# Kernel tuning notes

Hardware: AMD Instinct MI355X
Metric: run time of the kernel (lower is better)

Reference implementation:

```python
import jax, jax.numpy as jnp
import numpy as np

VOCAB = 1024
EMBED = 256
HIDDEN = 512
MAX_LEN = 32
TEMP = 1.0
BATCH = 2048


def setup_inputs() -> dict:
    key = jax.random.key(0)
    ks = jax.random.split(key, 11)
    s = 0.02  # small init scale for weights
    return dict(
        x=jax.random.normal(ks[0], (BATCH, HIDDEN), dtype=jnp.float32),
        gumbel=jax.random.gumbel(ks[1], (MAX_LEN, BATCH, VOCAB), dtype=jnp.float32),
        W_ih=jax.random.normal(ks[2], (4 * HIDDEN, EMBED), dtype=jnp.float32) * s,
        W_hh=jax.random.normal(ks[3], (4 * HIDDEN, HIDDEN), dtype=jnp.float32) * s,
        b_ih=jax.random.normal(ks[4], (4 * HIDDEN,), dtype=jnp.float32) * s,
        b_hh=jax.random.normal(ks[5], (4 * HIDDEN,), dtype=jnp.float32) * s,
        W_out=jax.random.normal(ks[6], (VOCAB, HIDDEN), dtype=jnp.float32) * s,
        b_out=jax.random.normal(ks[7], (VOCAB,), dtype=jnp.float32) * s,
        W_emb=jax.random.normal(ks[8], (EMBED, VOCAB), dtype=jnp.float32) * s,
        b_emb=jax.random.normal(ks[9], (EMBED,), dtype=jnp.float32) * s,
        sos=jax.random.normal(ks[10], (EMBED,), dtype=jnp.float32) * 0.01,
    )


def reference(x, gumbel, W_ih, W_hh, b_ih, b_hh, W_out, b_out, W_emb, b_emb, sos):
    B = x.shape[0]
    h0 = x                                   # prev_hidden = input features
    c0 = jnp.zeros_like(x)
    e0 = jnp.broadcast_to(sos, (B, EMBED))   # SOS embedding

    def step(carry, g):
        h, c, e = carry
        # torch LSTMCell gate order: i, f, g, o
        gates = e @ W_ih.T + b_ih + h @ W_hh.T + b_hh   # [B, 4H]
        i, f, gg, o = jnp.split(gates, 4, axis=-1)
        i = jax.nn.sigmoid(i)
        f = jax.nn.sigmoid(f)
        gg = jnp.tanh(gg)
        o = jax.nn.sigmoid(o)
        c_new = f * c + i * gg
        h_new = o * jnp.tanh(c_new)
        logits = h_new @ W_out.T + b_out                # [B, V]
        # RelaxedOneHotCategorical rsample: softmax((logits + Gumbel)/temp)
        x_s = jax.nn.softmax((logits + g) / TEMP, axis=-1)
        e_new = x_s @ W_emb.T + b_emb                   # [B, E]
        return (h_new, c_new, e_new), x_s

    _, seq = jax.lax.scan(step, (h0, c0, e0), gumbel)   # [L, B, V]
    seq = jnp.transpose(seq, (1, 0, 2))                 # [B, L, V]
    eos = jnp.zeros((B, 1, VOCAB), seq.dtype).at[:, 0, 0].set(1.0)
    return jnp.concatenate([seq, eos], axis=1)          # [B, L+1, V]
```

## Files before the change

kernel.cpp:

```cpp
#include <hip/hip_runtime.h>
#include <hip/hip_bf16.h>

#define B_   2048
#define V_   1024
#define H_   512
#define E_   256
#define L_   32

typedef __attribute__((ext_vector_type(4))) float f32x4;
typedef unsigned short u16;
typedef unsigned int   u32;
typedef unsigned char  u8;
typedef unsigned long long u64;
typedef long long      i64;

__device__ __forceinline__ u32 f32b(float x){ union{float f;u32 u;}v; v.f=x; return v.u; }
__device__ __forceinline__ float bf32(u32 u){ union{float f;u32 u;}v; v.u=u; return v.f; }
__device__ __forceinline__ u16 f2bf(float x) {
    u32 u = f32b(x);
    u32 r = u + 0x7fffu + ((u >> 16) & 1u);
    return (u16)(r >> 16);
}
__device__ __forceinline__ u8 f2e4m3(float x) {
    u32 u = f32b(x);
    u32 s = (u >> 24) & 0x80u;
    u32 a = u & 0x7fffffffu;
    if (a < 0x3c800000u) return (u8)s;
    if (a > 0x43e00000u) a = 0x43e00000u;
    u32 r = a + 0x000fffffu + ((a >> 20) & 1u);
    if (r > 0x43e00000u) r = 0x43e00000u;
    u32 ex = (r >> 23) - 120u;
    u32 mn = (r >> 20) & 7u;
    return (u8)(s | (ex << 3) | mn);
}
__device__ __forceinline__ u8 f2fp8(float x) {
#if __has_builtin(__builtin_amdgcn_cvt_pk_fp8_f32)
    return (u8)(__builtin_amdgcn_cvt_pk_fp8_f32(x, x, 0, false) & 0xff);
#else
    return f2e4m3(x);
#endif
}
__device__ __forceinline__ float sig_(float x)  { return 1.f / (1.f + __expf(-x)); }
__device__ __forceinline__ float tanh_(float x) { return 1.f - 2.f / (__expf(2.f * x) + 1.f); }

__device__ __forceinline__ void ag_st64(void* p, u64 v) {
    __hip_atomic_store((u64*)p, v, __ATOMIC_RELAXED, __HIP_MEMORY_SCOPE_AGENT);
}
__device__ __forceinline__ u64 ag_ld64(const void* p) {
    return __hip_atomic_load((const u64*)p, __ATOMIC_RELAXED, __HIP_MEMORY_SCOPE_AGENT);
}
__device__ __forceinline__ void ag_st32(void* p, u32 v) {
    __hip_atomic_store((u32*)p, v, __ATOMIC_RELAXED, __HIP_MEMORY_SCOPE_AGENT);
}
__device__ __forceinline__ u32 ag_ld32(const void* p) {
    return __hip_atomic_load((const u32*)p, __ATOMIC_RELAXED, __HIP_MEMORY_SCOPE_AGENT);
}

__global__ void prep(const float* __restrict__ W_ih, const float* __restrict__ W_hh,
                     const float* __restrict__ b_ih, const float* __restrict__ b_hh,
                     const float* __restrict__ W_out, const float* __restrict__ W_emb,
                     u8* __restrict__ w1f, u8* __restrict__ wof, u8* __restrict__ wef,
                     float* __restrict__ b1, u32* __restrict__ flg)
{
    int idx = blockIdx.x * 256 + threadIdx.x;
    if (idx < 1572864) {
        int e = idx & 7, l = (idx >> 3) & 63, jj = (idx >> 9) & 1, wv = (idx >> 10) & 7,
            g = (idx >> 13) & 3;
        int rest = idx >> 15;
        int hb = rest / 24, ks = rest % 24;
        int k = ks * 32 + ((l >> 4) << 3) + e;
        int row = g * 512 + hb * 256 + wv * 32 + jj * 16 + (l & 15);
        float v = (k < E_) ? W_ih[row * E_ + k] : W_hh[row * H_ + (k - E_)];
        w1f[idx] = f2e4m3(v * 64.f);
    } else if (idx < 2097152) {
        int j = idx - 1572864;
        int e = j & 7, l = (j >> 3) & 63, jj = (j >> 9) & 1, wv = (j >> 10) & 7,
            vh2 = (j >> 13) & 1, ks = (j >> 14) & 15, hb = j >> 18;
        int k = ks * 32 + ((l >> 4) << 3) + e;
        int v = hb * 512 + vh2 * 256 + wv * 32 + jj * 16 + (l & 15);
        wof[j] = f2e4m3(W_out[v * H_ + k] * 64.f);
    } else if (idx < 2359296) {
        int j = idx - 2097152;
        int e = j & 7, l = (j >> 3) & 63, jj = (j >> 9) & 1, wv = (j >> 10) & 7,
            ksp = (j >> 13) & 15, hb = j >> 17;
        int kv = hb * 512 + ksp * 32 + ((l >> 4) << 3) + e;
        int ce = wv * 32 + jj * 16 + (l & 15);
        wef[j] = f2e4m3(W_emb[ce * V_ + kv] * 64.f);
    } else if (idx < 2361344) {
        int j = idx - 2359296;
        b1[j] = b_ih[j] + b_hh[j];
    } else if (idx < 2365440) {
        flg[idx - 2361344] = 0u;
    }
}

#define AEO   131072u
#define XSO   143488u
#define RMX   151808u
#define RSM   152320u
#define LDS_TOTAL 152832

#define WAITVM_(N) asm volatile("s_waitcnt vmcnt(" #N ")" ::: "memory")
#define WAITVM(N) WAITVM_(N)

typedef const __attribute__((address_space(1))) void* gvp;
typedef __attribute__((address_space(3))) void* svp;

__device__ __forceinline__ void pbar(u32* myf, u32* pef, u32 n, u32 tid) {
    asm volatile("s_waitcnt vmcnt(0)" ::: "memory");
    __syncthreads();
    if (tid == 0) {
        __hip_atomic_fetch_add(myf, 1u, __ATOMIC_RELAXED, __HIP_MEMORY_SCOPE_AGENT);
        while (__hip_atomic_load(pef, __ATOMIC_RELAXED, __HIP_MEMORY_SCOPE_AGENT) < n)
            __builtin_amdgcn_s_sleep(2);
    }
    __syncthreads();
}

__global__ __launch_bounds__(512, 2)
void lstm_fused(const float* __restrict__ x, const float* __restrict__ gum,
                const u8* __restrict__ w1f, const u8* __restrict__ wof,
                const u8* __restrict__ wef, const float* __restrict__ b1,
                const float* __restrict__ b_out, const float* __restrict__ b_emb,
                const float* __restrict__ sos, float* __restrict__ out,
                u8* __restrict__ hx, char* __restrict__ ms, char* __restrict__ ep,
                u32* __restrict__ flg)
{
    extern __shared__ char smem[];

    const u32 tid = threadIdx.x;
    const u32 w   = tid >> 6;
    const u32 l   = tid & 63u;
    const u32 q   = l >> 4;
    const u32 col = l & 15u;

    const u32 bid = blockIdx.x;
    const u32 p   = bid & 127u;
    const u32 hb  = bid >> 7;
    const u32 ph  = 1u - hb;
    const int r0  = (int)(p << 4);

    u32* myf = flg + p * 32u + hb * 16u;
    u32* pef = flg + p * 32u + ph * 16u;
    u32 nbar = 0;

    const u32 wK  = w << 10;
    const u32 lB  = l << 4;
    const u32 l8  = l << 3;
    const u32 q8  = q << 3;
    const u32 colB776 = col * 776u;
    const u32 colB520 = col * 520u;

    const char* w1p = (const char*)w1f + (size_t)hb * 786432u;
    const char* wop = (const char*)wof + (size_t)hb * 262144u;
    const char* wep = (const char*)wef + (size_t)hb * 131072u;

#define ISS(BASE, C) do { u32 _c = (u32)(C); \
    u32 _o = (u32)__builtin_amdgcn_readfirstlane((int)(((_c & 15u) << 13) + wK)); \
    __builtin_amdgcn_global_load_lds((gvp)((BASE) + ((size_t)_c << 13) + wK + lB), \
                                     (svp)(smem + _o), 16, 0, 0); } while (0)

#define CONSA(G, C) { const char* _fb = smem + (((u32)(C) & 15u) << 13) + wK + l8; \
    acc[G][0] = __builtin_amdgcn_mfma_f32_16x16x32_fp8_fp8(a8, *(const i64*)(_fb), acc[G][0], 0, 0, 0); \
    acc[G][1] = __builtin_amdgcn_mfma_f32_16x16x32_fp8_fp8(a8, *(const i64*)(_fb + 512u), acc[G][1], 0, 0, 0); }

#define CONSB(V2, C, A8) { const char* _fb = smem + (((u32)(C) & 15u) << 13) + wK + l8; \
    accB[V2][0] = __builtin_amdgcn_mfma_f32_16x16x32_fp8_fp8(A8, *(const i64*)(_fb), accB[V2][0], 0, 0, 0); \
    accB[V2][1] = __builtin_amdgcn_mfma_f32_16x16x32_fp8_fp8(A8, *(const i64*)(_fb + 512u), accB[V2][1], 0, 0, 0); }

#define CONSC(C) { const char* _fb = smem + (((u32)(C) & 15u) << 13) + wK + l8; \
    i64 _x = *(const i64*)(smem + XSO + colB520 + (((u32)(C)) << 5) + q8); \
    accC[0] = __builtin_amdgcn_mfma_f32_16x16x32_fp8_fp8(_x, *(const i64*)(_fb), accC[0], 0, 0, 0); \
    accC[1] = __builtin_amdgcn_mfma_f32_16x16x32_fp8_fp8(_x, *(const i64*)(_fb + 512u), accC[1], 0, 0, 0); }

    for (u32 i = tid; i < 16u * 512u; i += 512u) {
        u32 row = i >> 9, vl = i & 511u;
        __builtin_nontemporal_store((hb == 0u && vl == 0u) ? 1.f : 0.f,
            &out[((size_t)(r0 + (int)row) * 33 + 32) * V_ + hb * 512u + vl]);
    }
    for (u32 i = tid; i < 16u * 256u; i += 512u) {
        u32 row = i >> 8, k = i & 255u;
        *(u8*)(smem + AEO + row * 776u + k) = f2fp8(sos[k] * 16.f);
    }
    for (u32 i = tid; i < 16u * 512u; i += 512u) {
        u32 row = i >> 9, k = i & 511u;
        *(u8*)(smem + AEO + row * 776u + 256u + k) = f2fp8(x[(r0 + (int)row) * H_ + k] * 16.f);
    }

    float bia[2], bfa[2], bga[2], boa[2];
    #pragma unroll
    for (int jj = 0; jj < 2; ++jj) {
        int jg = (int)(hb * 256u + (w << 5) + ((u32)jj << 4) + col);
        bia[jj] = b1[jg];           bfa[jj] = b1[H_ + jg];
        bga[jj] = b1[2 * H_ + jg];  boa[jj] = b1[3 * H_ + jg];
    }
    float bov[2][2];
    #pragma unroll
    for (int v2 = 0; v2 < 2; ++v2)
        #pragma unroll
        for (int jj = 0; jj < 2; ++jj)
            bov[v2][jj] = b_out[hb * 512u + (u32)v2 * 256u + (w << 5) + ((u32)jj << 4) + col];
    float bem16[2];
    #pragma unroll
    for (int jj = 0; jj < 2; ++jj)
        bem16[jj] = b_emb[(w << 5) + ((u32)jj << 4) + col] * 16.f;

    float creg[2][4];
    #pragma unroll
    for (int jj = 0; jj < 2; ++jj)
        #pragma unroll
        for (int r = 0; r < 4; ++r) creg[jj][r] = 0.f;

    __syncthreads();

    const f32x4 fz = {0.f, 0.f, 0.f, 0.f};
    const float S1 = 1.f / 1024.f;

    #pragma unroll 1
    for (int t = 0; t < L_; ++t) {
        f32x4 acc[4][2];
        #pragma unroll
        for (int g = 0; g < 4; ++g) { acc[g][0] = fz; acc[g][1] = fz; }

        ISS(w1p, 0);  ISS(w1p, 1);  ISS(w1p, 2);  ISS(w1p, 3);  ISS(w1p, 4);
        ISS(w1p, 5);  ISS(w1p, 6);  ISS(w1p, 7);  ISS(w1p, 8);  ISS(w1p, 9);
        ISS(w1p, 10); ISS(w1p, 11); ISS(w1p, 12); ISS(w1p, 13); ISS(w1p, 14);
        #pragma unroll 1
        for (int ks = 0; ks < 20; ++ks) {
            i64 a8 = *(const i64*)(smem + AEO + colB776 + ((u32)ks << 5) + q8);
            int c0 = ks << 2;
            WAITVM(11);
            CONSA(0, c0); CONSA(1, c0 + 1); CONSA(2, c0 + 2); CONSA(3, c0 + 3);
            ISS(w1p, c0 + 15); ISS(w1p, c0 + 16); ISS(w1p, c0 + 17); ISS(w1p, c0 + 18);
        }
        {   i64 a8 = *(const i64*)(smem + AEO + colB776 + (20u << 5) + q8);
            WAITVM(11); CONSA(0, 80); CONSA(1, 81); CONSA(2, 82); CONSA(3, 83); ISS(w1p, 95); }
        {   i64 a8 = *(const i64*)(smem + AEO + colB776 + (21u << 5) + q8);
            WAITVM(8);  CONSA(0, 84); CONSA(1, 85); CONSA(2, 86); CONSA(3, 87); }
        {   i64 a8 = *(const i64*)(smem + AEO + colB776 + (22u << 5) + q8);
            WAITVM(4);  CONSA(0, 88); CONSA(1, 89); CONSA(2, 90); CONSA(3, 91); }
        {   i64 a8 = *(const i64*)(smem + AEO + colB776 + (23u << 5) + q8);
            WAITVM(0);  CONSA(0, 92); CONSA(1, 93); CONSA(2, 94); CONSA(3, 95); }
        __syncthreads();

        #pragma unroll
        for (int jj = 0; jj < 2; ++jj) {
            u32 jg = hb * 256u + (w << 5) + ((u32)jj << 4) + col;
            #pragma unroll
            for (int r = 0; r < 4; ++r) {
                float gi = sig_(acc[0][jj][r] * S1 + bia[jj]);
                float gf = sig_(acc[1][jj][r] * S1 + bfa[jj]);
                float gg = tanh_(acc[2][jj][r] * S1 + bga[jj]);
                float go = sig_(acc[3][jj][r] * S1 + boa[jj]);
                float c  = gf * creg[jj][r] + gi * gg;
                creg[jj][r] = c;
                float h = go * tanh_(c);
                *(u8*)(smem + AEO + ((q << 2) + (u32)r) * 776u + 256u + jg) = f2fp8(h * 16.f);
            }
        }
        __syncthreads();

        {   u32 row = tid >> 5, off = (tid & 31u) << 3;
            u64 v = *(const u64*)(smem + AEO + row * 776u + 256u + hb * 256u + off);
            ag_st64(hx + (size_t)p * 8192u + row * 512u + hb * 256u + off, v);
        }
        ++nbar; pbar(myf, pef, nbar, tid);
        {   u32 row = tid >> 5, off = (tid & 31u) << 3;
            u64 v = ag_ld64(hx + (size_t)p * 8192u + row * 512u + ph * 256u + off);
            *(u64*)(smem + AEO + row * 776u + 256u + ph * 256u + off) = v;
        }
        __syncthreads();

        const float* gt = gum + (size_t)t * (B_ * V_) + (size_t)r0 * V_;
        float gr[2][2][4];
        #pragma unroll
        for (int v2 = 0; v2 < 2; ++v2)
            #pragma unroll
            for (int jj = 0; jj < 2; ++jj) {
                u32 vg = hb * 512u + (u32)v2 * 256u + (w << 5) + ((u32)jj << 4) + col;
                #pragma unroll
                for (int r = 0; r < 4; ++r)
                    gr[v2][jj][r] = __builtin_nontemporal_load(&gt[((q << 2) + (u32)r) * V_ + vg]);
            }

        f32x4 accB[2][2];
        accB[0][0] = fz; accB[0][1] = fz; accB[1][0] = fz; accB[1][1] = fz;
        ISS(wop, 0);  ISS(wop, 1);  ISS(wop, 2);  ISS(wop, 3);  ISS(wop, 4);
        ISS(wop, 5);  ISS(wop, 6);  ISS(wop, 7);  ISS(wop, 8);  ISS(wop, 9);
        ISS(wop, 10); ISS(wop, 11); ISS(wop, 12); ISS(wop, 13); ISS(wop, 14);
        #pragma unroll 1
        for (int g = 0; g < 4; ++g) {
            i64 a80 = *(const i64*)(smem + AEO + colB776 + 256u + (((u32)g << 1) << 5) + q8);
            i64 a81 = *(const i64*)(smem + AEO + colB776 + 256u + ((((u32)g << 1) | 1u) << 5) + q8);
            int c0 = g << 2;
            WAITVM(11);
            CONSB(0, c0, a80); CONSB(1, c0 + 1, a80);
            CONSB(0, c0 + 2, a81); CONSB(1, c0 + 3, a81);
            ISS(wop, c0 + 15); ISS(wop, c0 + 16); ISS(wop, c0 + 17); ISS(wop, c0 + 18);
        }
        {   i64 a80 = *(const i64*)(smem + AEO + colB776 + 256u + (8u << 5) + q8);
            i64 a81 = *(const i64*)(smem + AEO + colB776 + 256u + (9u << 5) + q8);
            WAITVM(11); CONSB(0, 16, a80); CONSB(1, 17, a80); CONSB(0, 18, a81); CONSB(1, 19, a81);
            ISS(wop, 31); }
        {   i64 a80 = *(const i64*)(smem + AEO + colB776 + 256u + (10u << 5) + q8);
            i64 a81 = *(const i64*)(smem + AEO + colB776 + 256u + (11u << 5) + q8);
            WAITVM(8);  CONSB(0, 20, a80); CONSB(1, 21, a80); CONSB(0, 22, a81); CONSB(1, 23, a81); }
        {   i64 a80 = *(const i64*)(smem + AEO + colB776 + 256u + (12u << 5) + q8);
            i64 a81 = *(const i64*)(smem + AEO + colB776 + 256u + (13u << 5) + q8);
            WAITVM(4);  CONSB(0, 24, a80); CONSB(1, 25, a80); CONSB(0, 26, a81); CONSB(1, 27, a81); }
        {   i64 a80 = *(const i64*)(smem + AEO + colB776 + 256u + (14u << 5) + q8);
            i64 a81 = *(const i64*)(smem + AEO + colB776 + 256u + (15u << 5) + q8);
            WAITVM(0);  CONSB(0, 28, a80); CONSB(1, 29, a80); CONSB(0, 30, a81); CONSB(1, 31, a81); }

        float m_loc[4], s_loc[4];
        #pragma unroll
        for (int r = 0; r < 4; ++r) m_loc[r] = -1e30f;
        #pragma unroll
        for (int v2 = 0; v2 < 2; ++v2)
            #pragma unroll
            for (int jj = 0; jj < 2; ++jj)
                #pragma unroll
                for (int r = 0; r < 4; ++r) {
                    float zz = accB[v2][jj][r] * S1 + bov[v2][jj] + gr[v2][jj][r];
                    accB[v2][jj][r] = zz;
                    m_loc[r] = fmaxf(m_loc[r], zz);
                }
        #pragma unroll
        for (int m = 1; m < 16; m <<= 1)
            #pragma unroll
            for (int r = 0; r < 4; ++r) m_loc[r] = fmaxf(m_loc[r], __shfl_xor(m_loc[r], m, 64));
        if (col == 0) {
            #pragma unroll
            for (int r = 0; r < 4; ++r)
                *(float*)(smem + RMX + ((((q << 2) + (u32)r) << 3) + w) * 4u) = m_loc[r];
        }
        __syncthreads();
        #pragma unroll
        for (int r = 0; r < 4; ++r) {
            float mm = -1e30f;
            #pragma unroll
            for (int ww = 0; ww < 8; ++ww)
                mm = fmaxf(mm, *(const float*)(smem + RMX + ((((q << 2) + (u32)r) << 3) + (u32)ww) * 4u));
            m_loc[r] = mm;
        }
        float ps[4] = {0.f, 0.f, 0.f, 0.f};
        #pragma unroll
        for (int v2 = 0; v2 < 2; ++v2)
            #pragma unroll
            for (int jj = 0; jj < 2; ++jj)
                #pragma unroll
                for (int r = 0; r < 4; ++r) {
                    float Ee = __expf(accB[v2][jj][r] - m_loc[r]);
                    accB[v2][jj][r] = Ee;
                    ps[r] += Ee;
                }
        #pragma unroll
        for (int m = 1; m < 16; m <<= 1)
            #pragma unroll
            for (int r = 0; r < 4; ++r) ps[r] += __shfl_xor(ps[r], m, 64);
        if (col == 0) {
            #pragma unroll
            for (int r = 0; r < 4; ++r)
                *(float*)(smem + RSM + ((((q << 2) + (u32)r) << 3) + w) * 4u) = ps[r];
        }
        __syncthreads();
        #pragma unroll
        for (int r = 0; r < 4; ++r) {
            float ss = 0.f;
            #pragma unroll
            for (int ww = 0; ww < 8; ++ww)
                ss += *(const float*)(smem + RSM + ((((q << 2) + (u32)r) << 3) + (u32)ww) * 4u);
            s_loc[r] = ss;
        }
        if (w == 0 && col == 0) {
            #pragma unroll
            for (int r = 0; r < 4; ++r) {
                u64 v = ((u64)f32b(s_loc[r]) << 32) | (u64)f32b(m_loc[r]);
                ag_st64(ms + (size_t)p * 256u + hb * 128u + (((q << 2) + (u32)r) << 3), v);
            }
        }
        ++nbar; pbar(myf, pef, nbar, tid);
        float fc[4], invs[4];
        #pragma unroll
        for (int r = 0; r < 4; ++r) {
            u64 v = ag_ld64(ms + (size_t)p * 256u + ph * 128u + (((q << 2) + (u32)r) << 3));
            float m_p = bf32((u32)v), s_p = bf32((u32)(v >> 32));
            float mg = fmaxf(m_loc[r], m_p);
            float f0 = __expf(m_loc[r] - mg);
            float s  = s_loc[r] * f0 + s_p * __expf(m_p - mg);
            fc[r] = f0; invs[r] = 1.f / s;
        }
        #pragma unroll
        for (int v2 = 0; v2 < 2; ++v2)
            #pragma unroll
            for (int jj = 0; jj < 2; ++jj) {
                u32 vl = (u32)v2 * 256u + (w << 5) + ((u32)jj << 4) + col;
                u32 vg = hb * 512u + vl;
                #pragma unroll
                for (int r = 0; r < 4; ++r) {
                    float Ee = accB[v2][jj][r] * fc[r];
                    *(u8*)(smem + XSO + ((q << 2) + (u32)r) * 520u + vl) = f2fp8(Ee * 256.f);
                    __builtin_nontemporal_store(Ee * invs[r],
                        &out[((size_t)(r0 + (int)((q << 2) + (u32)r)) * 33 + t) * V_ + vg]);
                }
            }
        __syncthreads();

        f32x4 accC[2];
        accC[0] = fz; accC[1] = fz;
        ISS(wep, 0);  ISS(wep, 1);  ISS(wep, 2);  ISS(wep, 3);  ISS(wep, 4);
        ISS(wep, 5);  ISS(wep, 6);  ISS(wep, 7);  ISS(wep, 8);  ISS(wep, 9);
        ISS(wep, 10); ISS(wep, 11); ISS(wep, 12); ISS(wep, 13); ISS(wep, 14);
        WAITVM(11); CONSC(0);  CONSC(1);  CONSC(2);  CONSC(3);  ISS(wep, 15);
        WAITVM(8);  CONSC(4);  CONSC(5);  CONSC(6);  CONSC(7);
        WAITVM(4);  CONSC(8);  CONSC(9);  CONSC(10); CONSC(11);
        WAITVM(0);  CONSC(12); CONSC(13); CONSC(14); CONSC(15);

        float part[2][4];
        #pragma unroll
        for (int jj = 0; jj < 2; ++jj)
            #pragma unroll
            for (int r = 0; r < 4; ++r)
                part[jj][r] = accC[jj][r] * invs[r] * (16.f / 16384.f);
        #pragma unroll
        for (int r = 0; r < 4; ++r) {
            u32 row = (q << 2) + (u32)r;
            u32 pv = (u32)f2bf(part[0][r]) | ((u32)f2bf(part[1][r]) << 16);
            ag_st32(ep + (size_t)p * 16384u + hb * 8192u + (((row << 3) + w) << 6) + (col << 2), pv);
        }
        ++nbar; pbar(myf, pef, nbar, tid);
        #pragma unroll
        for (int r = 0; r < 4; ++r) {
            u32 row = (q << 2) + (u32)r;
            u32 pv = ag_ld32(ep + (size_t)p * 16384u + ph * 8192u + (((row << 3) + w) << 6) + (col << 2));
            #pragma unroll
            for (int jj = 0; jj < 2; ++jj) {
                float pe = bf32(((pv >> (16 * jj)) & 0xffffu) << 16);
                float e16 = part[jj][r] + pe + bem16[jj];
                *(u8*)(smem + AEO + row * 776u + (w << 5) + ((u32)jj << 4) + col) = f2fp8(e16);
            }
        }
        __syncthreads();
    }
#undef ISS
#undef CONSA
#undef CONSB
#undef CONSC
}

extern "C" void kernel_launch(void* const* d_in, const int* in_sizes, int n_in,
                              void* d_out, int out_size, void* d_ws, size_t ws_size,
                              hipStream_t stream) {
    const float* x     = (const float*)d_in[0];
    const float* gum   = (const float*)d_in[1];
    const float* W_ih  = (const float*)d_in[2];
    const float* W_hh  = (const float*)d_in[3];
    const float* b_ih  = (const float*)d_in[4];
    const float* b_hh  = (const float*)d_in[5];
    const float* W_out = (const float*)d_in[6];
    const float* b_out = (const float*)d_in[7];
    const float* W_emb = (const float*)d_in[8];
    const float* b_emb = (const float*)d_in[9];
    const float* sos   = (const float*)d_in[10];
    float* out = (float*)d_out;

    char* ws = (char*)d_ws;
    u8*    w1f = (u8*)(ws);
    u8*    wof = (u8*)(ws + 1572864);
    u8*    wef = (u8*)(ws + 2097152);
    float* b1  = (float*)(ws + 2359296);
    u32*   flg = (u32*)(ws + 2367488);
    u8*    hx  = (u8*)(ws + 2383872);
    char*  ms  = (char*)(ws + 3432448);
    char*  ep  = (char*)(ws + 3465216);

    hipFuncSetAttribute((const void*)lstm_fused,
                        hipFuncAttributeMaxDynamicSharedMemorySize, LDS_TOTAL);

    prep<<<9240, 256, 0, stream>>>(W_ih, W_hh, b_ih, b_hh, W_out, W_emb,
                                   w1f, wof, wef, b1, flg);
    lstm_fused<<<256, 512, LDS_TOTAL, stream>>>(x, gum, w1f, wof, wef, b1,
                                                b_out, b_emb, sos, out,
                                                hx, ms, ep, flg);
}
```

Baseline: 962.2 us.

## Repartition LSTM across 4 blocks per 32-row group with a weight ring buffer

Each batch group now covers 32 rows split across 4 cooperating blocks instead of 16 rows across 2. Each block holds a quarter of the gate, output and embedding weights and reuses every weight fragment for two row tiles. Weights stream through a 12-slot LDS ring, and the next step's W1 prefetch is issued before the inter-block barrier. The softmax normalisation is deferred so one barrier per step replaces two, at the cost of a 4-way flag and partial-sum exchange.

```diff
diff --git a/kernel.cpp b/kernel.cpp
--- a/kernel.cpp
+++ b/kernel.cpp
@@ -62,60 +62,56 @@
                      u8* __restrict__ w1f, u8* __restrict__ wof, u8* __restrict__ wef,
                      float* __restrict__ b1, u32* __restrict__ flg)
 {
-    int idx = blockIdx.x * 256 + threadIdx.x;
-    if (idx < 1572864) {
-        int e = idx & 7, l = (idx >> 3) & 63, jj = (idx >> 9) & 1, wv = (idx >> 10) & 7,
-            g = (idx >> 13) & 3;
-        int rest = idx >> 15;
-        int hb = rest / 24, ks = rest % 24;
-        int k = ks * 32 + ((l >> 4) << 3) + e;
-        int row = g * 512 + hb * 256 + wv * 32 + jj * 16 + (l & 15);
-        float v = (k < E_) ? W_ih[row * E_ + k] : W_hh[row * H_ + (k - E_)];
+    u32 idx = blockIdx.x * 256 + threadIdx.x;
+    if (idx < 1572864u) {
+        u32 qb = idx / 393216u;
+        u32 r1 = idx - qb * 393216u;
+        u32 ks2 = r1 >> 15;
+        u32 r2 = r1 & 32767u;
+        u32 g = r2 >> 13, wv = (r2 >> 10) & 7u, s = (r2 >> 9) & 1u,
+            l = (r2 >> 3) & 63u, e = r2 & 7u;
+        u32 k = (2u * ks2 + s) * 32u + ((l >> 4) << 3) + e;
+        u32 n = g * 512u + qb * 128u + wv * 16u + (l & 15u);
+        float v = (k < E_) ? W_ih[n * E_ + k] : W_hh[n * H_ + (k - E_)];
         w1f[idx] = f2e4m3(v * 64.f);
-    } else if (idx < 2097152) {
-        int j = idx - 1572864;
-        int e = j & 7, l = (j >> 3) & 63, jj = (j >> 9) & 1, wv = (j >> 10) & 7,
-            vh2 = (j >> 13) & 1, ks = (j >> 14) & 15, hb = j >> 18;
-        int k = ks * 32 + ((l >> 4) << 3) + e;
-        int v = hb * 512 + vh2 * 256 + wv * 32 + jj * 16 + (l & 15);
+    } else if (idx < 2097152u) {
+        u32 j = idx - 1572864u;
+        u32 qb = j >> 17;
+        u32 rem = j & 131071u;
+        u32 ks = rem >> 13, wv = (rem >> 10) & 7u, jv = (rem >> 9) & 1u,
+            l = (rem >> 3) & 63u, e = rem & 7u;
+        u32 k = ks * 32u + ((l >> 4) << 3) + e;
+        u32 v = qb * 256u + wv * 32u + jv * 16u + (l & 15u);
         wof[j] = f2e4m3(W_out[v * H_ + k] * 64.f);
-    } else if (idx < 2359296) {
-        int j = idx - 2097152;
-        int e = j & 7, l = (j >> 3) & 63, jj = (j >> 9) & 1, wv = (j >> 10) & 7,
-            ksp = (j >> 13) & 15, hb = j >> 17;
-        int kv = hb * 512 + ksp * 32 + ((l >> 4) << 3) + e;
-        int ce = wv * 32 + jj * 16 + (l & 15);
+    } else if (idx < 2359296u) {
+        u32 j = idx - 2097152u;
+        u32 qb = j >> 16;
+        u32 rem = j & 65535u;
+        u32 ksp = rem >> 13, wv = (rem >> 10) & 7u, jc = (rem >> 9) & 1u,
+            l = (rem >> 3) & 63u, e = rem & 7u;
+        u32 kv = qb * 256u + ksp * 32u + ((l >> 4) << 3) + e;
+        u32 ce = wv * 32u + jc * 16u + (l & 15u);
         wef[j] = f2e4m3(W_emb[ce * V_ + kv] * 64.f);
-    } else if (idx < 2361344) {
-        int j = idx - 2359296;
+    } else if (idx < 2361344u) {
+        u32 j = idx - 2359296u;
         b1[j] = b_ih[j] + b_hh[j];
-    } else if (idx < 2365440) {
-        flg[idx - 2361344] = 0u;
+    } else if (idx < 2365440u) {
+        flg[idx - 2361344u] = 0u;
     }
 }
 
-#define AEO   131072u
-#define XSO   143488u
-#define RMX   151808u
-#define RSM   152320u
-#define LDS_TOTAL 152832
+#define RING  0u
+#define AEO   98304u
+#define XSO   123136u
+#define RMX   131584u
+#define RSM   132608u
+#define LDS_TOTAL 133632
 
 #define WAITVM_(N) asm volatile("s_waitcnt vmcnt(" #N ")" ::: "memory")
 #define WAITVM(N) WAITVM_(N)
 
 typedef const __attribute__((address_space(1))) void* gvp;
 typedef __attribute__((address_space(3))) void* svp;
-
-__device__ __forceinline__ void pbar(u32* myf, u32* pef, u32 n, u32 tid) {
-    asm volatile("s_waitcnt vmcnt(0)" ::: "memory");
-    __syncthreads();
-    if (tid == 0) {
-        __hip_atomic_fetch_add(myf, 1u, __ATOMIC_RELAXED, __HIP_MEMORY_SCOPE_AGENT);
-        while (__hip_atomic_load(pef, __ATOMIC_RELAXED, __HIP_MEMORY_SCOPE_AGENT) < n)
-            __builtin_amdgcn_s_sleep(2);
-    }
-    __syncthreads();
-}
 
 __global__ __launch_bounds__(512, 2)
 void lstm_fused(const float* __restrict__ x, const float* __restrict__ gum,
@@ -135,86 +131,107 @@
     const u32 col = l & 15u;
 
     const u32 bid = blockIdx.x;
-    const u32 p   = bid & 127u;
-    const u32 hb  = bid >> 7;
-    const u32 ph  = 1u - hb;
-    const int r0  = (int)(p << 4);
-
-    u32* myf = flg + p * 32u + hb * 16u;
-    u32* pef = flg + p * 32u + ph * 16u;
+    const u32 p   = bid & 63u;
+    const u32 qb  = bid >> 6;
+    const u32 q1  = (qb + 1u) & 3u, q2 = (qb + 2u) & 3u, q3 = (qb + 3u) & 3u;
+    const int r0  = (int)(p << 5);
+
+    u32* myf = flg + p * 64u + qb * 16u;
+    u32* pf0 = flg + p * 64u + q1 * 16u;
+    u32* pf1 = flg + p * 64u + q2 * 16u;
+    u32* pf2 = flg + p * 64u + q3 * 16u;
     u32 nbar = 0;
 
-    const u32 wK  = w << 10;
-    const u32 lB  = l << 4;
-    const u32 l8  = l << 3;
-    const u32 q8  = q << 3;
-    const u32 colB776 = col * 776u;
-    const u32 colB520 = col * 520u;
-
-    const char* w1p = (const char*)w1f + (size_t)hb * 786432u;
-    const char* wop = (const char*)wof + (size_t)hb * 262144u;
-    const char* wep = (const char*)wef + (size_t)hb * 131072u;
-
-#define ISS(BASE, C) do { u32 _c = (u32)(C); \
-    u32 _o = (u32)__builtin_amdgcn_readfirstlane((int)(((_c & 15u) << 13) + wK)); \
-    __builtin_amdgcn_global_load_lds((gvp)((BASE) + ((size_t)_c << 13) + wK + lB), \
+    const u32 wK = w << 10, lB = l << 4, l8 = l << 3, q8 = q << 3;
+    const char* w1q = (const char*)w1f + (size_t)qb * 393216u;
+    const char* woq = (const char*)wof + (size_t)qb * 131072u;
+    const char* weq = (const char*)wef + (size_t)qb * 65536u;
+
+#define PBAR() do { WAITVM(0); __syncthreads(); \
+    if (tid == 0) { \
+        __hip_atomic_fetch_add(myf, 1u, __ATOMIC_RELAXED, __HIP_MEMORY_SCOPE_AGENT); \
+        for (;;) { \
+            u32 _a = __hip_atomic_load(pf0, __ATOMIC_RELAXED, __HIP_MEMORY_SCOPE_AGENT); \
+            u32 _b = __hip_atomic_load(pf1, __ATOMIC_RELAXED, __HIP_MEMORY_SCOPE_AGENT); \
+            u32 _c = __hip_atomic_load(pf2, __ATOMIC_RELAXED, __HIP_MEMORY_SCOPE_AGENT); \
+            if (_a >= nbar && _b >= nbar && _c >= nbar) break; \
+            __builtin_amdgcn_s_sleep(2); \
+        } \
+    } \
+    __syncthreads(); } while (0)
+
+#define ISSR(BASE, GOFF, SOFF) do { \
+    u32 _o = (u32)__builtin_amdgcn_readfirstlane((int)((SOFF) + wK)); \
+    __builtin_amdgcn_global_load_lds((gvp)((BASE) + (size_t)(GOFF) + wK + lB), \
                                      (svp)(smem + _o), 16, 0, 0); } while (0)
-
-#define CONSA(G, C) { const char* _fb = smem + (((u32)(C) & 15u) << 13) + wK + l8; \
-    acc[G][0] = __builtin_amdgcn_mfma_f32_16x16x32_fp8_fp8(a8, *(const i64*)(_fb), acc[G][0], 0, 0, 0); \
-    acc[G][1] = __builtin_amdgcn_mfma_f32_16x16x32_fp8_fp8(a8, *(const i64*)(_fb + 512u), acc[G][1], 0, 0, 0); }
-
-#define CONSB(V2, C, A8) { const char* _fb = smem + (((u32)(C) & 15u) << 13) + wK + l8; \
-    accB[V2][0] = __builtin_amdgcn_mfma_f32_16x16x32_fp8_fp8(A8, *(const i64*)(_fb), accB[V2][0], 0, 0, 0); \
-    accB[V2][1] = __builtin_amdgcn_mfma_f32_16x16x32_fp8_fp8(A8, *(const i64*)(_fb + 512u), accB[V2][1], 0, 0, 0); }
-
-#define CONSC(C) { const char* _fb = smem + (((u32)(C) & 15u) << 13) + wK + l8; \
-    i64 _x = *(const i64*)(smem + XSO + colB520 + (((u32)(C)) << 5) + q8); \
-    accC[0] = __builtin_amdgcn_mfma_f32_16x16x32_fp8_fp8(_x, *(const i64*)(_fb), accC[0], 0, 0, 0); \
-    accC[1] = __builtin_amdgcn_mfma_f32_16x16x32_fp8_fp8(_x, *(const i64*)(_fb + 512u), accC[1], 0, 0, 0); }
-
-    for (u32 i = tid; i < 16u * 512u; i += 512u) {
-        u32 row = i >> 9, vl = i & 511u;
-        __builtin_nontemporal_store((hb == 0u && vl == 0u) ? 1.f : 0.f,
-            &out[((size_t)(r0 + (int)row) * 33 + 32) * V_ + hb * 512u + vl]);
+#define ISSL(BASE, C, SLOT) ISSR(BASE, (u32)(C) * 8192u, (u32)(SLOT) * 8192u)
+
+#define CONSA(G, SB, A00, A10, A01, A11) { \
+    const char* _fb = smem + (SB) + wK + l8; \
+    i64 _f0 = *(const i64*)(_fb); i64 _f1 = *(const i64*)(_fb + 512u); \
+    acc[G][0] = __builtin_amdgcn_mfma_f32_16x16x32_fp8_fp8(A00, _f0, acc[G][0], 0, 0, 0); \
+    acc[G][0] = __builtin_amdgcn_mfma_f32_16x16x32_fp8_fp8(A10, _f1, acc[G][0], 0, 0, 0); \
+    acc[G][1] = __builtin_amdgcn_mfma_f32_16x16x32_fp8_fp8(A01, _f0, acc[G][1], 0, 0, 0); \
+    acc[G][1] = __builtin_amdgcn_mfma_f32_16x16x32_fp8_fp8(A11, _f1, acc[G][1], 0, 0, 0); }
+
+#define CONSB(SB, A0, A1) { \
+    const char* _fb = smem + (SB) + wK + l8; \
+    i64 _g0 = *(const i64*)(_fb); i64 _g1 = *(const i64*)(_fb + 512u); \
+    accB[0][0] = __builtin_amdgcn_mfma_f32_16x16x32_fp8_fp8(A0, _g0, accB[0][0], 0, 0, 0); \
+    accB[1][0] = __builtin_amdgcn_mfma_f32_16x16x32_fp8_fp8(A0, _g1, accB[1][0], 0, 0, 0); \
+    accB[0][1] = __builtin_amdgcn_mfma_f32_16x16x32_fp8_fp8(A1, _g0, accB[0][1], 0, 0, 0); \
+    accB[1][1] = __builtin_amdgcn_mfma_f32_16x16x32_fp8_fp8(A1, _g1, accB[1][1], 0, 0, 0); }
+
+#define CONSC(SB, X0, X1) { \
+    const char* _fb = smem + (SB) + wK + l8; \
+    i64 _g0 = *(const i64*)(_fb); i64 _g1 = *(const i64*)(_fb + 512u); \
+    accC[0][0] = __builtin_amdgcn_mfma_f32_16x16x32_fp8_fp8(X0, _g0, accC[0][0], 0, 0, 0); \
+    accC[1][0] = __builtin_amdgcn_mfma_f32_16x16x32_fp8_fp8(X0, _g1, accC[1][0], 0, 0, 0); \
+    accC[0][1] = __builtin_amdgcn_mfma_f32_16x16x32_fp8_fp8(X1, _g0, accC[0][1], 0, 0, 0); \
+    accC[1][1] = __builtin_amdgcn_mfma_f32_16x16x32_fp8_fp8(X1, _g1, accC[1][1], 0, 0, 0); }
+
+#define BA8(KS, RT) (*(const i64*)(smem + AEO + (((RT)*16u + col) * 776u) + 256u + ((u32)(KS) << 5) + q8))
+#define XA8(KSP, RT) (*(const i64*)(smem + XSO + (((RT)*16u + col) * 264u) + ((u32)(KSP) << 5) + q8))
+
+    for (u32 i = tid; i < 32u * 256u; i += 512u) {
+        u32 row = i >> 8, vl = i & 255u;
+        __builtin_nontemporal_store((qb == 0u && vl == 0u) ? 1.f : 0.f,
+            &out[((size_t)(r0 + (int)row) * 33 + 32) * V_ + qb * 256u + vl]);
     }
-    for (u32 i = tid; i < 16u * 256u; i += 512u) {
+    for (u32 i = tid; i < 32u * 256u; i += 512u) {
         u32 row = i >> 8, k = i & 255u;
         *(u8*)(smem + AEO + row * 776u + k) = f2fp8(sos[k] * 16.f);
     }
-    for (u32 i = tid; i < 16u * 512u; i += 512u) {
+    for (u32 i = tid; i < 32u * 512u; i += 512u) {
         u32 row = i >> 9, k = i & 511u;
-        *(u8*)(smem + AEO + row * 776u + 256u + k) = f2fp8(x[(r0 + (int)row) * H_ + k] * 16.f);
+        *(u8*)(smem + AEO + row * 776u + 256u + k) = f2fp8(x[(r0 + (int)(row)) * H_ + k] * 16.f);
     }
 
-    float bia[2], bfa[2], bga[2], boa[2];
+    const u32 jg = qb * 128u + (w << 4) + col;
+    const float bi_ = b1[jg],            bf_ = b1[H_ + jg],
+                bg_ = b1[2 * H_ + jg],   bo_ = b1[3 * H_ + jg];
+    float bov[2], bem16[2];
     #pragma unroll
-    for (int jj = 0; jj < 2; ++jj) {
-        int jg = (int)(hb * 256u + (w << 5) + ((u32)jj << 4) + col);
-        bia[jj] = b1[jg];           bfa[jj] = b1[H_ + jg];
-        bga[jj] = b1[2 * H_ + jg];  boa[jj] = b1[3 * H_ + jg];
-    }
-    float bov[2][2];
+    for (int jv = 0; jv < 2; ++jv)
+        bov[jv] = b_out[qb * 256u + (w << 5) + (u32)jv * 16u + col];
     #pragma unroll
-    for (int v2 = 0; v2 < 2; ++v2)
-        #pragma unroll
-        for (int jj = 0; jj < 2; ++jj)
-            bov[v2][jj] = b_out[hb * 512u + (u32)v2 * 256u + (w << 5) + ((u32)jj << 4) + col];
-    float bem16[2];
-    #pragma unroll
-    for (int jj = 0; jj < 2; ++jj)
-        bem16[jj] = b_emb[(w << 5) + ((u32)jj << 4) + col] * 16.f;
+    for (int jc = 0; jc < 2; ++jc)
+        bem16[jc] = b_emb[(w << 5) + (u32)jc * 16u + col] * 16.f;
 
     float creg[2][4];
     #pragma unroll
-    for (int jj = 0; jj < 2; ++jj)
-        #pragma unroll
-        for (int r = 0; r < 4; ++r) creg[jj][r] = 0.f;
+    for (int rt = 0; rt < 2; ++rt)
+        #pragma unroll
+        for (int r = 0; r < 4; ++r) creg[rt][r] = 0.f;
 
     __syncthreads();
 
     const f32x4 fz = {0.f, 0.f, 0.f, 0.f};
     const float S1 = 1.f / 1024.f;
+
+    ISSL(w1q, 0, 0);  ISSL(w1q, 1, 1);  ISSL(w1q, 2, 2);  ISSL(w1q, 3, 3);
+    ISSL(w1q, 4, 4);  ISSL(w1q, 5, 5);  ISSL(w1q, 6, 6);  ISSL(w1q, 7, 7);
+    ISSL(w1q, 8, 8);  ISSL(w1q, 9, 9);  ISSL(w1q, 10, 10);
 
     #pragma unroll 1
     for (int t = 0; t < L_; ++t) {
@@ -222,230 +239,315 @@
         #pragma unroll
         for (int g = 0; g < 4; ++g) { acc[g][0] = fz; acc[g][1] = fz; }
 
-        ISS(w1p, 0);  ISS(w1p, 1);  ISS(w1p, 2);  ISS(w1p, 3);  ISS(w1p, 4);
-        ISS(w1p, 5);  ISS(w1p, 6);  ISS(w1p, 7);  ISS(w1p, 8);  ISS(w1p, 9);
-        ISS(w1p, 10); ISS(w1p, 11); ISS(w1p, 12); ISS(w1p, 13); ISS(w1p, 14);
+        u32 co = 0, io = 90112u, gio = 90112u;
         #pragma unroll 1
-        for (int ks = 0; ks < 20; ++ks) {
-            i64 a8 = *(const i64*)(smem + AEO + colB776 + ((u32)ks << 5) + q8);
-            int c0 = ks << 2;
-            WAITVM(11);
-            CONSA(0, c0); CONSA(1, c0 + 1); CONSA(2, c0 + 2); CONSA(3, c0 + 3);
-            ISS(w1p, c0 + 15); ISS(w1p, c0 + 16); ISS(w1p, c0 + 17); ISS(w1p, c0 + 18);
-        }
-        {   i64 a8 = *(const i64*)(smem + AEO + colB776 + (20u << 5) + q8);
-            WAITVM(11); CONSA(0, 80); CONSA(1, 81); CONSA(2, 82); CONSA(3, 83); ISS(w1p, 95); }
-        {   i64 a8 = *(const i64*)(smem + AEO + colB776 + (21u << 5) + q8);
-            WAITVM(8);  CONSA(0, 84); CONSA(1, 85); CONSA(2, 86); CONSA(3, 87); }
-        {   i64 a8 = *(const i64*)(smem + AEO + colB776 + (22u << 5) + q8);
-            WAITVM(4);  CONSA(0, 88); CONSA(1, 89); CONSA(2, 90); CONSA(3, 91); }
-        {   i64 a8 = *(const i64*)(smem + AEO + colB776 + (23u << 5) + q8);
-            WAITVM(0);  CONSA(0, 92); CONSA(1, 93); CONSA(2, 94); CONSA(3, 95); }
+        for (u32 ks2 = 0; ks2 < 9; ++ks2) {
+            u32 ab = AEO + col * 776u + (ks2 << 6);
+            i64 a00 = *(const i64*)(smem + ab + q8);
+            i64 a10 = *(const i64*)(smem + ab + 32u + q8);
+            i64 a01 = *(const i64*)(smem + ab + 12416u + q8);
+            i64 a11 = *(const i64*)(smem + ab + 12416u + 32u + q8);
+            #pragma unroll
+            for (int g = 0; g < 4; ++g) {
+                WAITVM(10);
+                CONSA(g, co, a00, a10, a01, a11);
+                ISSR(w1q, gio, io);
+                co += 8192u; if (co == 98304u) co = 0u;
+                io += 8192u; if (io == 98304u) io = 0u;
+                gio += 8192u;
+            }
+        }
+        {
+            u32 ab = AEO + col * 776u + (9u << 6);
+            i64 a00 = *(const i64*)(smem + ab + q8);
+            i64 a10 = *(const i64*)(smem + ab + 32u + q8);
+            i64 a01 = *(const i64*)(smem + ab + 12416u + q8);
+            i64 a11 = *(const i64*)(smem + ab + 12416u + 32u + q8);
+            WAITVM(10); CONSA(0, 0u,      a00, a10, a01, a11); ISSL(w1q, 47, 11);
+            WAITVM(10); CONSA(1, 8192u,   a00, a10, a01, a11);
+            WAITVM(9);  CONSA(2, 16384u,  a00, a10, a01, a11);
+            WAITVM(8);  CONSA(3, 24576u,  a00, a10, a01, a11);
+        }
+        {
+            u32 ab = AEO + col * 776u + (10u << 6);
+            i64 a00 = *(const i64*)(smem + ab + q8);
+            i64 a10 = *(const i64*)(smem + ab + 32u + q8);
+            i64 a01 = *(const i64*)(smem + ab + 12416u + q8);
+            i64 a11 = *(const i64*)(smem + ab + 12416u + 32u + q8);
+            WAITVM(7); CONSA(0, 32768u, a00, a10, a01, a11);
+            WAITVM(6); CONSA(1, 40960u, a00, a10, a01, a11);
+            WAITVM(5); CONSA(2, 49152u, a00, a10, a01, a11);
+            WAITVM(4); CONSA(3, 57344u, a00, a10, a01, a11);
+        }
+        {
+            u32 ab = AEO + col * 776u + (11u << 6);
+            i64 a00 = *(const i64*)(smem + ab + q8);
+            i64 a10 = *(const i64*)(smem + ab + 32u + q8);
+            i64 a01 = *(const i64*)(smem + ab + 12416u + q8);
+            i64 a11 = *(const i64*)(smem + ab + 12416u + 32u + q8);
+            WAITVM(3); CONSA(0, 65536u, a00, a10, a01, a11);
+            WAITVM(2); CONSA(1, 73728u, a00, a10, a01, a11);
+            WAITVM(1); CONSA(2, 81920u, a00, a10, a01, a11);
+            WAITVM(0); CONSA(3, 90112u, a00, a10, a01, a11);
+        }
         __syncthreads();
 
         #pragma unroll
-        for (int jj = 0; jj < 2; ++jj) {
-            u32 jg = hb * 256u + (w << 5) + ((u32)jj << 4) + col;
+        for (int rt = 0; rt < 2; ++rt)
             #pragma unroll
             for (int r = 0; r < 4; ++r) {
-                float gi = sig_(acc[0][jj][r] * S1 + bia[jj]);
-                float gf = sig_(acc[1][jj][r] * S1 + bfa[jj]);
-                float gg = tanh_(acc[2][jj][r] * S1 + bga[jj]);
-                float go = sig_(acc[3][jj][r] * S1 + boa[jj]);
-                float c  = gf * creg[jj][r] + gi * gg;
-                creg[jj][r] = c;
+                float gi = sig_(acc[0][rt][r] * S1 + bi_);
+                float gf = sig_(acc[1][rt][r] * S1 + bf_);
+                float gg = tanh_(acc[2][rt][r] * S1 + bg_);
+                float go = sig_(acc[3][rt][r] * S1 + bo_);
+                float c  = gf * creg[rt][r] + gi * gg;
+                creg[rt][r] = c;
                 float h = go * tanh_(c);
-                *(u8*)(smem + AEO + ((q << 2) + (u32)r) * 776u + 256u + jg) = f2fp8(h * 16.f);
-            }
-        }
+                u32 row = ((u32)rt << 4) + (q << 2) + (u32)r;
+                *(u8*)(smem + AEO + row * 776u + 256u + jg) = f2fp8(h * 16.f);
+            }
         __syncthreads();
 
-        {   u32 row = tid >> 5, off = (tid & 31u) << 3;
-            u64 v = *(const u64*)(smem + AEO + row * 776u + 256u + hb * 256u + off);
-            ag_st64(hx + (size_t)p * 8192u + row * 512u + hb * 256u + off, v);
-        }
-        ++nbar; pbar(myf, pef, nbar, tid);
-        {   u32 row = tid >> 5, off = (tid & 31u) << 3;
-            u64 v = ag_ld64(hx + (size_t)p * 8192u + row * 512u + ph * 256u + off);
-            *(u64*)(smem + AEO + row * 776u + 256u + ph * 256u + off) = v;
-        }
-        __syncthreads();
-
+        {   u32 row = tid >> 4, off = (tid & 15u) << 3;
+            u64 v = *(const u64*)(smem + AEO + row * 776u + 256u + qb * 128u + off);
+            ag_st64(hx + (size_t)p * 16384u + qb * 4096u + row * 128u + off, v);
+        }
+        ISSL(woq, 0, 0);  ISSL(woq, 1, 1);  ISSL(woq, 2, 2);  ISSL(woq, 3, 3);
+        ISSL(woq, 4, 4);  ISSL(woq, 5, 5);  ISSL(woq, 6, 6);  ISSL(woq, 7, 7);
+        ISSL(woq, 8, 8);  ISSL(woq, 9, 9);  ISSL(woq, 10, 10);
         const float* gt = gum + (size_t)t * (B_ * V_) + (size_t)r0 * V_;
         float gr[2][2][4];
         #pragma unroll
-        for (int v2 = 0; v2 < 2; ++v2)
-            #pragma unroll
-            for (int jj = 0; jj < 2; ++jj) {
-                u32 vg = hb * 512u + (u32)v2 * 256u + (w << 5) + ((u32)jj << 4) + col;
-                #pragma unroll
-                for (int r = 0; r < 4; ++r)
-                    gr[v2][jj][r] = __builtin_nontemporal_load(&gt[((q << 2) + (u32)r) * V_ + vg]);
-            }
+        for (int jv = 0; jv < 2; ++jv)
+            #pragma unroll
+            for (int rt = 0; rt < 2; ++rt) {
+                u32 vg = qb * 256u + (w << 5) + (u32)jv * 16u + col;
+                #pragma unroll
+                for (int r = 0; r < 4; ++r) {
+                    u32 row = ((u32)rt << 4) + (q << 2) + (u32)r;
+                    gr[jv][rt][r] = __builtin_nontemporal_load(&gt[row * V_ + vg]);
+                }
+            }
+        ++nbar; PBAR();
+
+        {   u32 row = tid >> 4, off = (tid & 15u) << 3;
+            u64 v1 = ag_ld64(hx + (size_t)p * 16384u + q1 * 4096u + row * 128u + off);
+            u64 v2 = ag_ld64(hx + (size_t)p * 16384u + q2 * 4096u + row * 128u + off);
+            u64 v3 = ag_ld64(hx + (size_t)p * 16384u + q3 * 4096u + row * 128u + off);
+            *(u64*)(smem + AEO + row * 776u + 256u + q1 * 128u + off) = v1;
+            *(u64*)(smem + AEO + row * 776u + 256u + q2 * 128u + off) = v2;
+            *(u64*)(smem + AEO + row * 776u + 256u + q3 * 128u + off) = v3;
+        }
+        __syncthreads();
 
         f32x4 accB[2][2];
         accB[0][0] = fz; accB[0][1] = fz; accB[1][0] = fz; accB[1][1] = fz;
-        ISS(wop, 0);  ISS(wop, 1);  ISS(wop, 2);  ISS(wop, 3);  ISS(wop, 4);
-        ISS(wop, 5);  ISS(wop, 6);  ISS(wop, 7);  ISS(wop, 8);  ISS(wop, 9);
-        ISS(wop, 10); ISS(wop, 11); ISS(wop, 12); ISS(wop, 13); ISS(wop, 14);
-        #pragma unroll 1
-        for (int g = 0; g < 4; ++g) {
-            i64 a80 = *(const i64*)(smem + AEO + colB776 + 256u + (((u32)g << 1) << 5) + q8);
-            i64 a81 = *(const i64*)(smem + AEO + colB776 + 256u + ((((u32)g << 1) | 1u) << 5) + q8);
-            int c0 = g << 2;
-            WAITVM(11);
-            CONSB(0, c0, a80); CONSB(1, c0 + 1, a80);
-            CONSB(0, c0 + 2, a81); CONSB(1, c0 + 3, a81);
-            ISS(wop, c0 + 15); ISS(wop, c0 + 16); ISS(wop, c0 + 17); ISS(wop, c0 + 18);
-        }
-        {   i64 a80 = *(const i64*)(smem + AEO + colB776 + 256u + (8u << 5) + q8);
-            i64 a81 = *(const i64*)(smem + AEO + colB776 + 256u + (9u << 5) + q8);
-            WAITVM(11); CONSB(0, 16, a80); CONSB(1, 17, a80); CONSB(0, 18, a81); CONSB(1, 19, a81);
-            ISS(wop, 31); }
-        {   i64 a80 = *(const i64*)(smem + AEO + colB776 + 256u + (10u << 5) + q8);
-            i64 a81 = *(const i64*)(smem + AEO + colB776 + 256u + (11u << 5) + q8);
-            WAITVM(8);  CONSB(0, 20, a80); CONSB(1, 21, a80); CONSB(0, 22, a81); CONSB(1, 23, a81); }
-        {   i64 a80 = *(const i64*)(smem + AEO + colB776 + 256u + (12u << 5) + q8);
-            i64 a81 = *(const i64*)(smem + AEO + colB776 + 256u + (13u << 5) + q8);
-            WAITVM(4);  CONSB(0, 24, a80); CONSB(1, 25, a80); CONSB(0, 26, a81); CONSB(1, 27, a81); }
-        {   i64 a80 = *(const i64*)(smem + AEO + colB776 + 256u + (14u << 5) + q8);
-            i64 a81 = *(const i64*)(smem + AEO + colB776 + 256u + (15u << 5) + q8);
-            WAITVM(0);  CONSB(0, 28, a80); CONSB(1, 29, a80); CONSB(0, 30, a81); CONSB(1, 31, a81); }
-
-        float m_loc[4], s_loc[4];
-        #pragma unroll
-        for (int r = 0; r < 4; ++r) m_loc[r] = -1e30f;
-        #pragma unroll
-        for (int v2 = 0; v2 < 2; ++v2)
-            #pragma unroll
-            for (int jj = 0; jj < 2; ++jj)
-                #pragma unroll
-                for (int r = 0; r < 4; ++r) {
-                    float zz = accB[v2][jj][r] * S1 + bov[v2][jj] + gr[v2][jj][r];
-                    accB[v2][jj][r] = zz;
-                    m_loc[r] = fmaxf(m_loc[r], zz);
+        { i64 a0 = BA8(0,0),  a1 = BA8(0,1);  WAITVM(10); CONSB(0u,      a0, a1); ISSL(woq, 11, 11); }
+        { i64 a0 = BA8(1,0),  a1 = BA8(1,1);  WAITVM(10); CONSB(8192u,   a0, a1); ISSL(woq, 12, 0); }
+        { i64 a0 = BA8(2,0),  a1 = BA8(2,1);  WAITVM(10); CONSB(16384u,  a0, a1); ISSL(woq, 13, 1); }
+        { i64 a0 = BA8(3,0),  a1 = BA8(3,1);  WAITVM(10); CONSB(24576u,  a0, a1); ISSL(woq, 14, 2); }
+        { i64 a0 = BA8(4,0),  a1 = BA8(4,1);  WAITVM(10); CONSB(32768u,  a0, a1); ISSL(woq, 15, 3); }
+        { i64 a0 = BA8(5,0),  a1 = BA8(5,1);  WAITVM(10); CONSB(40960u,  a0, a1); }
+        { i64 a0 = BA8(6,0),  a1 = BA8(6,1);  WAITVM(9);  CONSB(49152u,  a0, a1); }
+        { i64 a0 = BA8(7,0),  a1 = BA8(7,1);  WAITVM(8);  CONSB(57344u,  a0, a1); }
+        { i64 a0 = BA8(8,0),  a1 = BA8(8,1);  WAITVM(7);  CONSB(65536u,  a0, a1); }
+        { i64 a0 = BA8(9,0),  a1 = BA8(9,1);  WAITVM(6);  CONSB(73728u,  a0, a1); }
+        { i64 a0 = BA8(10,0), a1 = BA8(10,1); WAITVM(5);  CONSB(81920u,  a0, a1); }
+        { i64 a0 = BA8(11,0), a1 = BA8(11,1); WAITVM(4);  CONSB(90112u,  a0, a1); }
+        { i64 a0 = BA8(12,0), a1 = BA8(12,1); WAITVM(3);  CONSB(0u,      a0, a1); }
+        { i64 a0 = BA8(13,0), a1 = BA8(13,1); WAITVM(2);  CONSB(8192u,   a0, a1); }
+        { i64 a0 = BA8(14,0), a1 = BA8(14,1); WAITVM(1);  CONSB(16384u,  a0, a1); }
+        { i64 a0 = BA8(15,0), a1 = BA8(15,1); WAITVM(0);  CONSB(24576u,  a0, a1); }
+
+        float m_loc[2][4], s_loc[2][4];
+        #pragma unroll
+        for (int rt = 0; rt < 2; ++rt)
+            #pragma unroll
+            for (int r = 0; r < 4; ++r) m_loc[rt][r] = -1e30f;
+        #pragma unroll
+        for (int jv = 0; jv < 2; ++jv)
+            #pragma unroll
+            for (int rt = 0; rt < 2; ++rt)
+                #pragma unroll
+                for (int r = 0; r < 4; ++r) {
+                    float zz = accB[jv][rt][r] * S1 + bov[jv] + gr[jv][rt][r];
+                    accB[jv][rt][r] = zz;
+                    m_loc[rt][r] = fmaxf(m_loc[rt][r], zz);
                 }
         #pragma unroll
         for (int m = 1; m < 16; m <<= 1)
             #pragma unroll
-            for (int r = 0; r < 4; ++r) m_loc[r] = fmaxf(m_loc[r], __shfl_xor(m_loc[r], m, 64));
+            for (int rt = 0; rt < 2; ++rt)
+                #pragma unroll
+                for (int r = 0; r < 4; ++r)
+                    m_loc[rt][r] = fmaxf(m_loc[rt][r], __shfl_xor(m_loc[rt][r], m, 64));
         if (col == 0) {
             #pragma unroll
-            for (int r = 0; r < 4; ++r)
-                *(float*)(smem + RMX + ((((q << 2) + (u32)r) << 3) + w) * 4u) = m_loc[r];
+            for (int rt = 0; rt < 2; ++rt)
+                #pragma unroll
+                for (int r = 0; r < 4; ++r) {
+                    u32 row = ((u32)rt << 4) + (q << 2) + (u32)r;
+                    *(float*)(smem + RMX + (row * 8u + w) * 4u) = m_loc[rt][r];
+                }
         }
         __syncthreads();
         #pragma unroll
-        for (int r = 0; r < 4; ++r) {
-            float mm = -1e30f;
-            #pragma unroll
-            for (int ww = 0; ww < 8; ++ww)
-                mm = fmaxf(mm, *(const float*)(smem + RMX + ((((q << 2) + (u32)r) << 3) + (u32)ww) * 4u));
-            m_loc[r] = mm;
-        }
-        float ps[4] = {0.f, 0.f, 0.f, 0.f};
-        #pragma unroll
-        for (int v2 = 0; v2 < 2; ++v2)
-            #pragma unroll
-            for (int jj = 0; jj < 2; ++jj)
-                #pragma unroll
-                for (int r = 0; r < 4; ++r) {
-                    float Ee = __expf(accB[v2][jj][r] - m_loc[r]);
-                    accB[v2][jj][r] = Ee;
-                    ps[r] += Ee;
-                }
+        for (int rt = 0; rt < 2; ++rt)
+            #pragma unroll
+            for (int r = 0; r < 4; ++r) {
+                u32 row = ((u32)rt << 4) + (q << 2) + (u32)r;
+                float mm = -1e30f;
+                #pragma unroll
+                for (int ww = 0; ww < 8; ++ww)
+                    mm = fmaxf(mm, *(const float*)(smem + RMX + (row * 8u + (u32)ww) * 4u));
+                m_loc[rt][r] = mm;
+            }
+        ISSL(weq, 0, 0); ISSL(weq, 1, 1); ISSL(weq, 2, 2); ISSL(weq, 3, 3);
+        ISSL(weq, 4, 4); ISSL(weq, 5, 5); ISSL(weq, 6, 6); ISSL(weq, 7, 7);
+        float ps[2][4];
+        #pragma unroll
+        for (int rt = 0; rt < 2; ++rt)
+            #pragma unroll
+            for (int r = 0; r < 4; ++r) ps[rt][r] = 0.f;
+        #pragma unroll
+        for (int jv = 0; jv < 2; ++jv)
+            #pragma unroll
+            for (int rt = 0; rt < 2; ++rt) {
+                u32 vl = (w << 5) + (u32)jv * 16u + col;
+                #pragma unroll
+                for (int r = 0; r < 4; ++r) {
+                    float Ee = __expf(accB[jv][rt][r] - m_loc[rt][r]);
+                    accB[jv][rt][r] = Ee;
+                    ps[rt][r] += Ee;
+                    u32 row = ((u32)rt << 4) + (q << 2) + (u32)r;
+                    *(u8*)(smem + XSO + row * 264u + vl) = f2fp8(Ee * 256.f);
+                }
+            }
         #pragma unroll
         for (int m = 1; m < 16; m <<= 1)
             #pragma unroll
-            for (int r = 0; r < 4; ++r) ps[r] += __shfl_xor(ps[r], m, 64);
+            for (int rt = 0; rt < 2; ++rt)
+                #pragma unroll
+                for (int r = 0; r < 4; ++r)
+                    ps[rt][r] += __shfl_xor(ps[rt][r], m, 64);
         if (col == 0) {
             #pragma unroll
-            for (int r = 0; r < 4; ++r)
-                *(float*)(smem + RSM + ((((q << 2) + (u32)r) << 3) + w) * 4u) = ps[r];
+            for (int rt = 0; rt < 2; ++rt)
+                #pragma unroll
+                for (int r = 0; r < 4; ++r) {
+                    u32 row = ((u32)rt << 4) + (q << 2) + (u32)r;
+                    *(float*)(smem + RSM + (row * 8u + w) * 4u) = ps[rt][r];
+                }
         }
         __syncthreads();
         #pragma unroll
-        for (int r = 0; r < 4; ++r) {
-            float ss = 0.f;
-            #pragma unroll
-            for (int ww = 0; ww < 8; ++ww)
-                ss += *(const float*)(smem + RSM + ((((q << 2) + (u32)r) << 3) + (u32)ww) * 4u);
-            s_loc[r] = ss;
-        }
+        for (int rt = 0; rt < 2; ++rt)
+            #pragma unroll
+            for (int r = 0; r < 4; ++r) {
+                u32 row = ((u32)rt << 4) + (q << 2) + (u32)r;
+                float ss = 0.f;
+                #pragma unroll
+                for (int ww = 0; ww < 8; ++ww)
+                    ss += *(const float*)(smem + RSM + (row * 8u + (u32)ww) * 4u);
+                s_loc[rt][r] = ss;
+            }
+
+        f32x4 accC[2][2];
+        accC[0][0] = fz; accC[0][1] = fz; accC[1][0] = fz; accC[1][1] = fz;
+        { i64 x0 = XA8(0,0), x1 = XA8(0,1); WAITVM(7); CONSC(0u,      x0, x1); }
+        { i64 x0 = XA8(1,0), x1 = XA8(1,1); WAITVM(6); CONSC(8192u,   x0, x1); }
+        { i64 x0 = XA8(2,0), x1 = XA8(2,1); WAITVM(5); CONSC(16384u,  x0, x1); }
+        { i64 x0 = XA8(3,0), x1 = XA8(3,1); WAITVM(4); CONSC(24576u,  x0, x1); }
+        { i64 x0 = XA8(4,0), x1 = XA8(4,1); WAITVM(3); CONSC(32768u,  x0, x1); }
+        { i64 x0 = XA8(5,0), x1 = XA8(5,1); WAITVM(2); CONSC(40960u,  x0, x1); }
+        { i64 x0 = XA8(6,0), x1 = XA8(6,1); WAITVM(1); CONSC(49152u,  x0, x1); }
+        { i64 x0 = XA8(7,0), x1 = XA8(7,1); WAITVM(0); CONSC(57344u,  x0, x1); }
+
+        float part[2][2][4];
+        #pragma unroll
+        for (int jc = 0; jc < 2; ++jc)
+            #pragma unroll
+            for (int rt = 0; rt < 2; ++rt)
+                #pragma unroll
+                for (int r = 0; r < 4; ++r)
+                    part[jc][rt][r] = accC[jc][rt][r] * (16.f / 16384.f);
         if (w == 0 && col == 0) {
             #pragma unroll
+            for (int rt = 0; rt < 2; ++rt)
+                #pragma unroll
+                for (int r = 0; r < 4; ++r) {
+                    u32 row = ((u32)rt << 4) + (q << 2) + (u32)r;
+                    u64 v = ((u64)f32b(s_loc[rt][r]) << 32) | (u64)f32b(m_loc[rt][r]);
+                    ag_st64(ms + (size_t)p * 1024u + row * 32u + qb * 8u, v);
+                }
+        }
+        #pragma unroll
+        for (int rt = 0; rt < 2; ++rt)
+            #pragma unroll
             for (int r = 0; r < 4; ++r) {
-                u64 v = ((u64)f32b(s_loc[r]) << 32) | (u64)f32b(m_loc[r]);
-                ag_st64(ms + (size_t)p * 256u + hb * 128u + (((q << 2) + (u32)r) << 3), v);
-            }
-        }
-        ++nbar; pbar(myf, pef, nbar, tid);
-        float fc[4], invs[4];
-        #pragma unroll
-        for (int r = 0; r < 4; ++r) {
-            u64 v = ag_ld64(ms + (size_t)p * 256u + ph * 128u + (((q << 2) + (u32)r) << 3));
-            float m_p = bf32((u32)v), s_p = bf32((u32)(v >> 32));
-            float mg = fmaxf(m_loc[r], m_p);
-            float f0 = __expf(m_loc[r] - mg);
-            float s  = s_loc[r] * f0 + s_p * __expf(m_p - mg);
-            fc[r] = f0; invs[r] = 1.f / s;
-        }
-        #pragma unroll
-        for (int v2 = 0; v2 < 2; ++v2)
-            #pragma unroll
-            for (int jj = 0; jj < 2; ++jj) {
-                u32 vl = (u32)v2 * 256u + (w << 5) + ((u32)jj << 4) + col;
-                u32 vg = hb * 512u + vl;
-                #pragma unroll
-                for (int r = 0; r < 4; ++r) {
-                    float Ee = accB[v2][jj][r] * fc[r];
-                    *(u8*)(smem + XSO + ((q << 2) + (u32)r) * 520u + vl) = f2fp8(Ee * 256.f);
-                    __builtin_nontemporal_store(Ee * invs[r],
-                        &out[((size_t)(r0 + (int)((q << 2) + (u32)r)) * 33 + t) * V_ + vg]);
-                }
-            }
-        __syncthreads();
-
-        f32x4 accC[2];
-        accC[0] = fz; accC[1] = fz;
-        ISS(wep, 0);  ISS(wep, 1);  ISS(wep, 2);  ISS(wep, 3);  ISS(wep, 4);
-        ISS(wep, 5);  ISS(wep, 6);  ISS(wep, 7);  ISS(wep, 8);  ISS(wep, 9);
-        ISS(wep, 10); ISS(wep, 11); ISS(wep, 12); ISS(wep, 13); ISS(wep, 14);
-        WAITVM(11); CONSC(0);  CONSC(1);  CONSC(2);  CONSC(3);  ISS(wep, 15);
-        WAITVM(8);  CONSC(4);  CONSC(5);  CONSC(6);  CONSC(7);
-        WAITVM(4);  CONSC(8);  CONSC(9);  CONSC(10); CONSC(11);
-        WAITVM(0);  CONSC(12); CONSC(13); CONSC(14); CONSC(15);
-
-        float part[2][4];
-        #pragma unroll
-        for (int jj = 0; jj < 2; ++jj)
-            #pragma unroll
-            for (int r = 0; r < 4; ++r)
-                part[jj][r] = accC[jj][r] * invs[r] * (16.f / 16384.f);
-        #pragma unroll
-        for (int r = 0; r < 4; ++r) {
-            u32 row = (q << 2) + (u32)r;
-            u32 pv = (u32)f2bf(part[0][r]) | ((u32)f2bf(part[1][r]) << 16);
-            ag_st32(ep + (size_t)p * 16384u + hb * 8192u + (((row << 3) + w) << 6) + (col << 2), pv);
-        }
-        ++nbar; pbar(myf, pef, nbar, tid);
-        #pragma unroll
-        for (int r = 0; r < 4; ++r) {
-            u32 row = (q << 2) + (u32)r;
-            u32 pv = ag_ld32(ep + (size_t)p * 16384u + ph * 8192u + (((row << 3) + w) << 6) + (col << 2));
-            #pragma unroll
-            for (int jj = 0; jj < 2; ++jj) {
-                float pe = bf32(((pv >> (16 * jj)) & 0xffffu) << 16);
-                float e16 = part[jj][r] + pe + bem16[jj];
-                *(u8*)(smem + AEO + row * 776u + (w << 5) + ((u32)jj << 4) + col) = f2fp8(e16);
-            }
-        }
+                u32 row = ((u32)rt << 4) + (q << 2) + (u32)r;
+                u32 pv = (u32)f2bf(part[0][rt][r]) | ((u32)f2bf(part[1][rt][r]) << 16);
+                ag_st32(ep + (size_t)p * 65536u + qb * 16384u + ((row * 8u + w) * 16u + col) * 4u, pv);
+            }
+        ISSL(w1q, 0, 0);  ISSL(w1q, 1, 1);  ISSL(w1q, 2, 2);  ISSL(w1q, 3, 3);
+        ISSL(w1q, 4, 4);  ISSL(w1q, 5, 5);  ISSL(w1q, 6, 6);  ISSL(w1q, 7, 7);
+        ISSL(w1q, 8, 8);  ISSL(w1q, 9, 9);  ISSL(w1q, 10, 10);
+        ++nbar; PBAR();
+
+        float foinv[2][4];
+        #pragma unroll
+        for (int rt = 0; rt < 2; ++rt)
+            #pragma unroll
+            for (int r = 0; r < 4; ++r) {
+                u32 row = ((u32)rt << 4) + (q << 2) + (u32)r;
+                u64 v1 = ag_ld64(ms + (size_t)p * 1024u + row * 32u + q1 * 8u);
+                u64 v2 = ag_ld64(ms + (size_t)p * 1024u + row * 32u + q2 * 8u);
+                u64 v3 = ag_ld64(ms + (size_t)p * 1024u + row * 32u + q3 * 8u);
+                float m1 = bf32((u32)v1), s1 = bf32((u32)(v1 >> 32));
+                float m2 = bf32((u32)v2), s2 = bf32((u32)(v2 >> 32));
+                float m3 = bf32((u32)v3), s3 = bf32((u32)(v3 >> 32));
+                float m0 = m_loc[rt][r], s0 = s_loc[rt][r];
+                float mg = fmaxf(fmaxf(m0, m1), fmaxf(m2, m3));
+                float f0 = __expf(m0 - mg), f1 = __expf(m1 - mg),
+                      f2 = __expf(m2 - mg), f3 = __expf(m3 - mg);
+                float inv = 1.f / (s0 * f0 + s1 * f1 + s2 * f2 + s3 * f3);
+                foinv[rt][r] = f0 * inv;
+                u32 eoff = ((row * 8u + w) * 16u + col) * 4u;
+                u32 p1 = ag_ld32(ep + (size_t)p * 65536u + q1 * 16384u + eoff);
+                u32 p2 = ag_ld32(ep + (size_t)p * 65536u + q2 * 16384u + eoff);
+                u32 p3 = ag_ld32(ep + (size_t)p * 65536u + q3 * 16384u + eoff);
+                #pragma unroll
+                for (int jc = 0; jc < 2; ++jc) {
+                    float e1 = bf32(((p1 >> (16 * jc)) & 0xffffu) << 16);
+                    float e2 = bf32(((p2 >> (16 * jc)) & 0xffffu) << 16);
+                    float e3 = bf32(((p3 >> (16 * jc)) & 0xffffu) << 16);
+                    float e16 = (part[jc][rt][r] * f0 + e1 * f1 + e2 * f2 + e3 * f3) * inv
+                                + bem16[jc];
+                    *(u8*)(smem + AEO + row * 776u + (w << 5) + (u32)jc * 16u + col) = f2fp8(e16);
+                }
+            }
+        #pragma unroll
+        for (int jv = 0; jv < 2; ++jv)
+            #pragma unroll
+            for (int rt = 0; rt < 2; ++rt) {
+                u32 vg = qb * 256u + (w << 5) + (u32)jv * 16u + col;
+                #pragma unroll
+                for (int r = 0; r < 4; ++r) {
+                    u32 row = ((u32)rt << 4) + (q << 2) + (u32)r;
+                    __builtin_nontemporal_store(accB[jv][rt][r] * foinv[rt][r],
+                        &out[((size_t)(r0 + (int)row) * 33 + t) * V_ + vg]);
+                }
+            }
         __syncthreads();
     }
-#undef ISS
+#undef PBAR
+#undef ISSR
+#undef ISSL
 #undef CONSA
 #undef CONSB
 #undef CONSC
+#undef BA8
+#undef XA8
 }
 
 extern "C" void kernel_launch(void* const* d_in, const int* in_sizes, int n_in,
@@ -472,7 +574,7 @@
     u32*   flg = (u32*)(ws + 2367488);
     u8*    hx  = (u8*)(ws + 2383872);
     char*  ms  = (char*)(ws + 3432448);
-    char*  ep  = (char*)(ws + 3465216);
+    char*  ep  = (char*)(ws + 3497984);
 
     hipFuncSetAttribute((const void*)lstm_fused,
                         hipFuncAttributeMaxDynamicSharedMemorySize, LDS_TOTAL);
```

Result: slower. 1.229 ms (+27.7%).
